# Kernel tuning notes

Measured on AMD Instinct MI355X. Metric: run time of the kernel, lower is better.

Reference implementation:

```python
import jax, jax.numpy as jnp
import numpy as np

L = 2          # num layers
HID = 96       # hidden channels per layer


def _gate_conv(x, w, bias):
    # x: [B, Cin, H, W], w: [4*HID, Cin, 3, 3] -> [B, 4*HID, H, W], SAME padding
    y = jax.lax.conv_general_dilated(
        x, w, window_strides=(1, 1), padding='SAME',
        dimension_numbers=('NCHW', 'OIHW', 'NCHW'))
    return y + bias[None, :, None, None]


def setup_inputs() -> dict:
    key = jax.random.key(0)
    k_inp, k_w = jax.random.split(key)
    B, T, C, H, Wd = 8, 12, 96, 48, 48
    inp = jax.random.normal(k_inp, (B, T, C, H, Wd), dtype=jnp.float32)
    h0 = jnp.zeros((L, B, HID, H, Wd), dtype=jnp.float32)
    c0 = jnp.zeros((L, B, HID, H, Wd), dtype=jnp.float32)
    # gate conv weights: per layer [4*HID, C + HID, 3, 3] (fan-in scaled)
    W = jax.random.normal(k_w, (L, 4 * HID, C + HID, 3, 3), dtype=jnp.float32)
    W = W * (1.0 / np.sqrt((C + HID) * 9)).astype(np.float32)
    b = jnp.zeros((L, 4 * HID), dtype=jnp.float32)
    return {'inp': inp, 'h0': h0, 'c0': c0, 'W': W, 'b': b}


def reference(inp, h0, c0, W, b):
    # inp: [B,T,C,H,W]; h0,c0: [L,B,HID,H,W]; W: [L,4H,C+H,3,3]; b: [L,4H]
    xs = jnp.moveaxis(inp, 1, 0)  # [T,B,C,H,W]

    def step(carry, x_t):
        h, c = carry  # each [L,B,HID,H,W]
        layer_in = x_t
        new_h, new_c = [], []
        for l in range(L):
            z = jnp.concatenate([layer_in, h[l]], axis=1)  # [B, C+HID, H, W]
            gates = _gate_conv(z, W[l], b[l])              # [B, 4*HID, H, W]
            i, f, o, g = jnp.split(gates, 4, axis=1)
            c_n = jax.nn.sigmoid(f) * c[l] + jax.nn.sigmoid(i) * jnp.tanh(g)
            h_n = jax.nn.sigmoid(o) * jnp.tanh(c_n)
            new_h.append(h_n)
            new_c.append(c_n)
            layer_in = h_n
        h = jnp.stack(new_h)
        c = jnp.stack(new_c)
        return (h, c), h

    (h_f, c_f), hs = jax.lax.scan(step, (h0, c0), xs)
    # hs: [T,L,B,HID,H,W] -> all hidden states per layer, batch_first
    all_hidden = jnp.moveaxis(jnp.moveaxis(hs, 1, 0), 2, 1)  # [L,B,T,HID,H,W]
    return all_hidden, h_f, c_f
```

## Files before the change

### kernel.cpp

```cpp
#include <hip/hip_runtime.h>
#include <hip/hip_bf16.h>
#include <stdint.h>

#define HWDIM 48
#define PLANE 2304
#define NB 8
#define NT 12
#define CHID 96
#define OC 384
#define KTOT 1728
#define BN 144
#define NBLK_JOB 128
#define NCHUNK 54
#define PPLANE 2500
#define PGRP 3
#define IMG_E ((size_t)PGRP * PPLANE * 32)
#define SLOT_E ((size_t)NB * IMG_E)
#define BT ((size_t)CHID * PLANE)

typedef __attribute__((ext_vector_type(8))) short short8;
typedef __attribute__((ext_vector_type(4))) float f32x4;
typedef __attribute__((ext_vector_type(4))) unsigned int u32x4;

__device__ __forceinline__ unsigned short f2bf(float f) {
  union { float f; uint32_t u; } x; x.f = f;
  uint32_t u = x.u;
  return (unsigned short)((u + 0x7FFFu + ((u >> 16) & 1u)) >> 16);
}

__global__ void convlstm_wconv(const float* __restrict__ W, unsigned short* __restrict__ Wb, int total) {
  int idx = blockIdx.x * 256 + threadIdx.x;
  if (idx >= total) return;
  const int PER_L = NCHUNK * 24 * 64 * 8;
  int layer = idx / PER_L;
  int r = idx - layer * PER_L;
  int jj = r & 7;
  int l = (r >> 3) & 63;
  int fr = r >> 9;
  int rm = fr % 24;
  int c = fr / 24;
  int oc = rm * 16 + (l & 15);
  int k = c * 32 + ((l >> 4) << 3) + jj;
  int tap = k / 192;
  int ic = k - tap * 192;
  float v = W[(((size_t)layer * OC + oc) * 192 + ic) * 9 + tap];
  Wb[idx] = f2bf(v);
}

__global__ void pack_interior(const float* __restrict__ src, unsigned short* __restrict__ dst,
                              int mode, int t_base, int slot_mask) {
  __shared__ float T[32][65];
  int bid = blockIdx.x;
  int tile = bid % 36;
  int grp  = (bid / 36) % 3;
  int imgi = bid / 108;
  int slot; size_t srcoff;
  if (mode == 0) {
    int b = imgi & 7; int t = t_base + (imgi >> 3);
    srcoff = ((size_t)b * NT + t) * BT;
    slot = (t & slot_mask) * NB + b;
  } else {
    int b = imgi & 7; int l = imgi >> 3;
    srcoff = (size_t)imgi * BT;
    slot = (l * 2 + 1) * NB + b;
  }
  const float* s = src + srcoff + (size_t)grp * 32 * PLANE + tile * 64;
  const int tid = threadIdx.x;
#pragma unroll
  for (int r = 0; r < 8; ++r) {
    int ch = r * 4 + (tid >> 6);
    T[ch][tid & 63] = s[(size_t)ch * PLANE + (tid & 63)];
  }
  __syncthreads();
  int p = tid >> 2, sq = tid & 3;
  int pos = tile * 64 + p;
  int py = pos / 48 + 1, px = pos % 48 + 1;
  unsigned short v[8];
#pragma unroll
  for (int i = 0; i < 8; ++i) v[i] = f2bf(T[sq * 8 + i][p]);
  *(short8*)(dst + ((size_t)slot * PGRP + grp) * (PPLANE * 32) + (py * 50 + px) * 32 + sq * 8) = *(short8*)v;
}

__global__ void border_zero(unsigned short* dst, int nplanes) {
  int idx = blockIdx.x * 256 + threadIdx.x;
  if (idx >= nplanes * 784) return;
  int plane = idx / 784;
  int r = idx - plane * 784;
  int g = r >> 2, sq = r & 3;
  int py, px;
  if (g < 50)       { py = 0;       px = g; }
  else if (g < 100) { py = 49;      px = g - 50; }
  else if (g < 148) { py = g - 99;  px = 0; }
  else              { py = g - 147; px = 49; }
  u32x4 z = {0, 0, 0, 0};
  *(u32x4*)(dst + (size_t)plane * (PPLANE * 32) + (py * 50 + px) * 32 + sq * 8) = z;
}

struct Job {
  const unsigned short* xp;
  const unsigned short* hp;
  unsigned short* hw;
  const short8* w;
  const float* bias;
  float* c_base;
  float* h_out; long long ho_bs;
  float* hf;
};

__global__ __launch_bounds__(512, 1) void convlstm_step(Job j0, Job j1) {
  __shared__ __align__(16) char smem[96000];
  unsigned short* HALO = (unsigned short*)smem;
  float* GL = (float*)smem;
  unsigned short* HP = (unsigned short*)(smem + 26112);

  const int tid = threadIdx.x;
  const Job j = (blockIdx.x < NBLK_JOB) ? j0 : j1;
  const int n0 = (blockIdx.x % NBLK_JOB) * BN;
  const int lane = tid & 63;
  const int wid = tid >> 6;
  const int g = wid & 3;
  const int h2 = wid >> 2;

  const int bb = n0 / PLANE;
  const int spb = n0 - bb * PLANE;
  const int y0 = spb / 48;

  const unsigned short* xb = j.xp + (size_t)bb * IMG_E;
  const unsigned short* hb = j.hp + (size_t)bb * IMG_E;
  for (int it = 0; it < 3; ++it) {
    int pg = tid + it * 512;
    if (pg < 1500) {
      int tensor = pg / 750;
      int rem = pg - tensor * 750;
      int grp = rem / 250;
      int r2 = rem - grp * 250;
      int rr = r2 / 50;
      int px = r2 - rr * 50;
      int gs = tensor * 3 + grp;
      const unsigned short* src = (tensor ? hb : xb) + (size_t)grp * (PPLANE * 32)
                                  + (size_t)((y0 + rr) * 50 + px) * 32;
#pragma unroll
      for (int q = 0; q < 4; ++q) {
        short8 v = *(const short8*)(src + q * 8);
        *(short8*)&HALO[(size_t)(((gs * 4 + q) * 5 + rr) * 50 + px) * 8] = v;
      }
    }
  }

  f32x4 acc[3][9];
#pragma unroll
  for (int rm = 0; rm < 3; ++rm) {
    f32x4 bi = *(const f32x4*)(j.bias + g * 96 + h2 * 48 + rm * 16 + ((lane >> 4) << 2));
#pragma unroll
    for (int cn = 0; cn < 9; ++cn) acc[rm][cn] = bi;
  }

  const short8* aw = j.w + (size_t)(g * 6 + h2 * 3) * 64 + lane;
  short8 a_cur[3];
#pragma unroll
  for (int rm = 0; rm < 3; ++rm) a_cur[rm] = aw[rm * 64];

  __syncthreads();

  const int lofs = (lane >> 4) * 2000 + (lane & 15) * 8;

  auto bload = [&](int c, short8* bf) {
    const int tap = c / 6, gs2 = c - tap * 6;
    const int kh = tap / 3, kw = tap - kh * 3;
#pragma unroll
    for (int cn = 0; cn < 9; ++cn) {
      const int off = gs2 * 8000 + ((cn / 3) + kh) * 400 + ((cn % 3) * 16 + kw) * 8 + lofs;
      bf[cn] = *(const short8*)&HALO[off];
    }
  };

  short8 b_cur[9];
  bload(0, b_cur);

#pragma unroll 1
  for (int c = 0; c < NCHUNK; ++c) {
    const int c1 = (c + 1 < NCHUNK) ? (c + 1) : (NCHUNK - 1);
    short8 a_nxt[3];
#pragma unroll
    for (int rm = 0; rm < 3; ++rm) a_nxt[rm] = aw[(size_t)c1 * 1536 + rm * 64];
    short8 b_nxt[9];
    bload(c1, b_nxt);

#pragma unroll
    for (int cn = 0; cn < 9; ++cn)
#pragma unroll
      for (int rm = 0; rm < 3; ++rm)
        acc[rm][cn] = __builtin_amdgcn_mfma_f32_16x16x32_bf16(a_cur[rm], b_cur[cn], acc[rm][cn], 0, 0, 0);

#pragma unroll
    for (int rm = 0; rm < 3; ++rm) a_cur[rm] = a_nxt[rm];
#pragma unroll
    for (int cn = 0; cn < 9; ++cn) b_cur[cn] = b_nxt[cn];
  }

#pragma unroll
  for (int cc = 0; cc < 9; ++cc) {
    __syncthreads();
#pragma unroll
    for (int rm = 0; rm < 3; ++rm)
#pragma unroll
      for (int r = 0; r < 4; ++r)
        GL[(g * 96 + h2 * 48 + rm * 16 + ((lane >> 4) << 2) + r) * 17 + (lane & 15)] = acc[rm][cc][r];
    __syncthreads();

    const int colL = tid & 15;
    const int chb = (tid >> 4) * 3;
    const int spe = spb + cc * 16 + colL;
    float* cb_ = j.c_base + (size_t)bb * (CHID * PLANE) + spe;
    float* hb_ = j.h_out + (size_t)bb * j.ho_bs + spe;
    float* hf_ = j.hf ? (j.hf + (size_t)bb * (CHID * PLANE) + spe) : nullptr;
#pragma unroll
    for (int q = 0; q < 3; ++q) {
      const int ch = chb + q;
      const float gi = GL[(0 * 96 + ch) * 17 + colL];
      const float gf = GL[(1 * 96 + ch) * 17 + colL];
      const float go = GL[(2 * 96 + ch) * 17 + colL];
      const float gg = GL[(3 * 96 + ch) * 17 + colL];
      const float si = 1.f / (1.f + __expf(-gi));
      const float sf = 1.f / (1.f + __expf(-gf));
      const float so = 1.f / (1.f + __expf(-go));
      const float e2g = __expf(2.f * gg);
      const float tg = 1.f - 2.f / (e2g + 1.f);
      const float cold = cb_[(size_t)ch * PLANE];
      const float cn2 = sf * cold + si * tg;
      const float e2c = __expf(2.f * cn2);
      const float tc = 1.f - 2.f / (e2c + 1.f);
      const float hn = so * tc;
      cb_[(size_t)ch * PLANE] = cn2;
      hb_[(size_t)ch * PLANE] = hn;
      if (hf_) hf_[(size_t)ch * PLANE] = hn;
      HP[(cc * 16 + colL) * 96 + ch] = f2bf(hn);
    }
  }
  __syncthreads();

#pragma unroll
  for (int it = 0; it < 4; ++it) {
    int gi = tid + it * 512;
    if (gi < 1728) {
      int gq = gi / 144;
      int p  = gi - gq * 144;
      int grp = gq >> 2, sq = gq & 3;
      int pos = spb + p;
      int py = pos / 48 + 1, px = pos % 48 + 1;
      short8 v = *(short8*)&HP[p * 96 + grp * 32 + sq * 8];
      *(short8*)(j.hw + (size_t)bb * IMG_E + (size_t)grp * (PPLANE * 32) + (py * 50 + px) * 32 + sq * 8) = v;
    }
  }
}

extern "C" void kernel_launch(void* const* d_in, const int* in_sizes, int n_in,
                              void* d_out, int out_size, void* d_ws, size_t ws_size,
                              hipStream_t stream) {
  const float* inp  = (const float*)d_in[0];
  const float* h0   = (const float*)d_in[1];
  const float* c0   = (const float*)d_in[2];
  const float* W    = (const float*)d_in[3];
  const float* bias = (const float*)d_in[4];

  float* AH = (float*)d_out;
  float* HF = AH + (size_t)2 * NB * NT * BT;
  float* CF = HF + (size_t)2 * NB * BT;

  const size_t WB_BYTES = (size_t)2 * NCHUNK * 24 * 64 * 8 * 2;
  const size_t PH_BYTES = (size_t)4 * SLOT_E * 2;
  const size_t PX_BIG   = (size_t)NT * SLOT_E * 2;
  const bool big = ws_size >= WB_BYTES + PH_BYTES + PX_BIG;
  unsigned short* Wb = (unsigned short*)d_ws;
  unsigned short* ph = (unsigned short*)((char*)d_ws + WB_BYTES);
  unsigned short* px = (unsigned short*)((char*)d_ws + WB_BYTES + PH_BYTES);

  {
    int total = 2 * NCHUNK * 24 * 64 * 8;
    convlstm_wconv<<<(total + 255) / 256, 256, 0, stream>>>(W, Wb, total);
  }
  {
    int np_ph = 4 * NB * 3;
    border_zero<<<(np_ph * 784 + 255) / 256, 256, 0, stream>>>(ph, np_ph);
    int np_px = (big ? NT : 2) * NB * 3;
    border_zero<<<(np_px * 784 + 255) / 256, 256, 0, stream>>>(px, np_px);
  }
  {
    int n_img = big ? (NT * NB) : (2 * NB);
    pack_interior<<<n_img * 108, 256, 0, stream>>>(inp, px, 0, 0, big ? 15 : 1);
    pack_interior<<<2 * NB * 108, 256, 0, stream>>>(h0, ph, 1, 0, 0);
  }
  hipMemcpyAsync(CF, c0, (size_t)2 * NB * BT * sizeof(float), hipMemcpyDeviceToDevice, stream);

  const size_t PER_L = (size_t)NCHUNK * 24 * 64;

  auto mkjob = [&](int l, int t) -> Job {
    Job j;
    if (l == 0) j.xp = px + (size_t)(big ? t : (t & 1)) * SLOT_E;
    else        j.xp = ph + (size_t)(0 * 2 + (t & 1)) * SLOT_E;
    j.hp = ph + (size_t)(l * 2 + ((t + 1) & 1)) * SLOT_E;
    j.hw = ph + (size_t)(l * 2 + (t & 1)) * SLOT_E;
    j.w = (const short8*)Wb + (size_t)l * PER_L;
    j.bias = bias + l * OC;
    j.c_base = CF + (size_t)l * NB * BT;
    j.h_out = AH + (size_t)l * NB * NT * BT + (size_t)t * BT;
    j.ho_bs = (long long)NT * BT;
    j.hf = (t == NT - 1) ? (HF + (size_t)l * NB * BT) : nullptr;
    return j;
  };

  for (int k = 0; k <= NT; ++k) {
    const bool hasA = (k <= NT - 1);
    const bool hasB = (k >= 1);
    Job ja, jb;
    int njobs = 0;
    if (hasA) { ja = mkjob(0, k); njobs = 1; }
    if (hasB) {
      Job xj = mkjob(1, k - 1);
      if (njobs) jb = xj; else ja = xj;
      njobs++;
    }
    if (njobs == 1) jb = ja;
    convlstm_step<<<njobs * NBLK_JOB, 512, 0, stream>>>(ja, jb);
    if (!big && k + 2 <= NT - 1)
      pack_interior<<<NB * 108, 256, 0, stream>>>(inp, px, 0, k + 2, 1);
  }
}
```

Measured before the change: 784.3 us.

## Interleave gate weight rows so LSTM epilogue runs from registers without LDS transpose

Output channels of the gate weights are reordered during conversion so each MFMA accumulator's four rows hold the i,f,o,g gates of one hidden channel. The epilogue then computes the LSTM cell update straight from accumulator registers. This removes the nine LDS staging rounds and their barriers, and the bias load is remapped to match. It also raises wave priority around the MFMA block. The cost is less coalesced global c/h access, since each lane now touches 16-wide column strips per channel.

```diff
diff --git a/kernel.cpp b/kernel.cpp
--- a/kernel.cpp
+++ b/kernel.cpp
@@ -40,10 +40,11 @@
   int rm = fr % 24;
   int c = fr / 24;
   int oc = rm * 16 + (l & 15);
+  int oco = (oc & 3) * 96 + (oc >> 2);
   int k = c * 32 + ((l >> 4) << 3) + jj;
   int tap = k / 192;
   int ic = k - tap * 192;
-  float v = W[(((size_t)layer * OC + oc) * 192 + ic) * 9 + tap];
+  float v = W[(((size_t)layer * OC + oco) * 192 + ic) * 9 + tap];
   Wb[idx] = f2bf(v);
 }
 
@@ -110,16 +111,13 @@
 __global__ __launch_bounds__(512, 1) void convlstm_step(Job j0, Job j1) {
   __shared__ __align__(16) char smem[96000];
   unsigned short* HALO = (unsigned short*)smem;
-  float* GL = (float*)smem;
-  unsigned short* HP = (unsigned short*)(smem + 26112);
+  unsigned short* HP = (unsigned short*)smem;
 
   const int tid = threadIdx.x;
   const Job j = (blockIdx.x < NBLK_JOB) ? j0 : j1;
   const int n0 = (blockIdx.x % NBLK_JOB) * BN;
   const int lane = tid & 63;
   const int wid = tid >> 6;
-  const int g = wid & 3;
-  const int h2 = wid >> 2;
 
   const int bb = n0 / PLANE;
   const int spb = n0 - bb * PLANE;
@@ -150,12 +148,15 @@
   f32x4 acc[3][9];
 #pragma unroll
   for (int rm = 0; rm < 3; ++rm) {
-    f32x4 bi = *(const f32x4*)(j.bias + g * 96 + h2 * 48 + rm * 16 + ((lane >> 4) << 2));
+    const int ch = wid * 12 + rm * 4 + (lane >> 4);
+    f32x4 bi;
+#pragma unroll
+    for (int r = 0; r < 4; ++r) bi[r] = j.bias[r * 96 + ch];
 #pragma unroll
     for (int cn = 0; cn < 9; ++cn) acc[rm][cn] = bi;
   }
 
-  const short8* aw = j.w + (size_t)(g * 6 + h2 * 3) * 64 + lane;
+  const short8* aw = j.w + (size_t)(wid * 3) * 64 + lane;
   short8 a_cur[3];
 #pragma unroll
   for (int rm = 0; rm < 3; ++rm) a_cur[rm] = aw[rm * 64];
@@ -186,11 +187,13 @@
     short8 b_nxt[9];
     bload(c1, b_nxt);
 
+    __builtin_amdgcn_s_setprio(1);
 #pragma unroll
     for (int cn = 0; cn < 9; ++cn)
 #pragma unroll
       for (int rm = 0; rm < 3; ++rm)
         acc[rm][cn] = __builtin_amdgcn_mfma_f32_16x16x32_bf16(a_cur[rm], b_cur[cn], acc[rm][cn], 0, 0, 0);
+    __builtin_amdgcn_s_setprio(0);
 
 #pragma unroll
     for (int rm = 0; rm < 3; ++rm) a_cur[rm] = a_nxt[rm];
@@ -198,43 +201,36 @@
     for (int cn = 0; cn < 9; ++cn) b_cur[cn] = b_nxt[cn];
   }
 
-#pragma unroll
-  for (int cc = 0; cc < 9; ++cc) {
-    __syncthreads();
-#pragma unroll
-    for (int rm = 0; rm < 3; ++rm)
-#pragma unroll
-      for (int r = 0; r < 4; ++r)
-        GL[(g * 96 + h2 * 48 + rm * 16 + ((lane >> 4) << 2) + r) * 17 + (lane & 15)] = acc[rm][cc][r];
-    __syncthreads();
-
-    const int colL = tid & 15;
-    const int chb = (tid >> 4) * 3;
-    const int spe = spb + cc * 16 + colL;
-    float* cb_ = j.c_base + (size_t)bb * (CHID * PLANE) + spe;
-    float* hb_ = j.h_out + (size_t)bb * j.ho_bs + spe;
-    float* hf_ = j.hf ? (j.hf + (size_t)bb * (CHID * PLANE) + spe) : nullptr;
-#pragma unroll
-    for (int q = 0; q < 3; ++q) {
-      const int ch = chb + q;
-      const float gi = GL[(0 * 96 + ch) * 17 + colL];
-      const float gf = GL[(1 * 96 + ch) * 17 + colL];
-      const float go = GL[(2 * 96 + ch) * 17 + colL];
-      const float gg = GL[(3 * 96 + ch) * 17 + colL];
+  __syncthreads();
+
+#pragma unroll
+  for (int rm = 0; rm < 3; ++rm) {
+    const int ch = wid * 12 + rm * 4 + (lane >> 4);
+    float* cb_ = j.c_base + (size_t)bb * (CHID * PLANE) + (size_t)ch * PLANE;
+    float* hb_ = j.h_out + (size_t)bb * j.ho_bs + (size_t)ch * PLANE;
+    float* hf_ = j.hf ? (j.hf + (size_t)bb * (CHID * PLANE) + (size_t)ch * PLANE) : nullptr;
+#pragma unroll
+    for (int cn = 0; cn < 9; ++cn) {
+      const int col = cn * 16 + (lane & 15);
+      const int spe = spb + col;
+      const float gi = acc[rm][cn][0];
+      const float gf = acc[rm][cn][1];
+      const float go = acc[rm][cn][2];
+      const float gg = acc[rm][cn][3];
       const float si = 1.f / (1.f + __expf(-gi));
       const float sf = 1.f / (1.f + __expf(-gf));
       const float so = 1.f / (1.f + __expf(-go));
       const float e2g = __expf(2.f * gg);
       const float tg = 1.f - 2.f / (e2g + 1.f);
-      const float cold = cb_[(size_t)ch * PLANE];
+      const float cold = cb_[spe];
       const float cn2 = sf * cold + si * tg;
       const float e2c = __expf(2.f * cn2);
       const float tc = 1.f - 2.f / (e2c + 1.f);
       const float hn = so * tc;
-      cb_[(size_t)ch * PLANE] = cn2;
-      hb_[(size_t)ch * PLANE] = hn;
-      if (hf_) hf_[(size_t)ch * PLANE] = hn;
-      HP[(cc * 16 + colL) * 96 + ch] = f2bf(hn);
+      cb_[spe] = cn2;
+      hb_[spe] = hn;
+      if (hf_) hf_[spe] = hn;
+      HP[col * 96 + ch] = f2bf(hn);
     }
   }
   __syncthreads();
```

Result: faster. 679.9 us (-13.3%).
